# Performance work log

Hardware: AMD Instinct MI355X
Metric: run time of the kernel (lower is better)

Reference implementation:

```python
import jax, jax.numpy as jnp
import numpy as np

B, S, F = 4, 2048, 256
H, D = 8, 32            # n_heads, width_embedding; H*D == F
LN_EPS = 1e-3           # tf.keras LayerNormalization default epsilon


def setup_inputs() -> dict:
    key = jax.random.key(0)
    ks = jax.random.split(key, 6)
    s = 1.0 / np.sqrt(F)
    return {
        "x": jax.random.normal(ks[0], (B, S, F), dtype=jnp.float32),
        "Wq": jax.random.normal(ks[1], (F, H * D), dtype=jnp.float32) * s,
        "Wk": jax.random.normal(ks[2], (F, H * D), dtype=jnp.float32) * s,
        "Wv": jax.random.normal(ks[3], (F, H * D), dtype=jnp.float32) * s,
        "Wf": jax.random.normal(ks[4], (H * D, F), dtype=jnp.float32) * s,
        "bf": jnp.zeros((F,), dtype=jnp.float32),
    }


def reference(x, Wq, Wk, Wv, Wf, bf):
    # QKV projections (no bias), split heads: [B,S,H*D] -> [B,H,S,D]
    def split(t):
        return t.reshape(B, S, H, D).transpose(0, 2, 1, 3)

    q = split(x @ Wq) / jnp.sqrt(jnp.asarray(H, x.dtype))  # NOTE: module scales by sqrt(n_heads)
    k = split(x @ Wk)
    v = split(x @ Wv)

    scores = jnp.einsum("bhsd,bhtd->bhst", q, k)          # [B,H,S,S]
    attn = jax.nn.softmax(scores, axis=-1)
    ctx = jnp.einsum("bhst,bhtd->bhsd", attn, v)           # [B,H,S,D]

    y = ctx.transpose(0, 2, 1, 3).reshape(B, S, H * D)     # merge heads
    y = jax.nn.relu(y @ Wf + bf)                            # final dense with relu

    # residual + LayerNorm(center=False, scale=False)
    z = x + y
    mean = jnp.mean(z, axis=-1, keepdims=True)
    var = jnp.var(z, axis=-1, keepdims=True)
    return (z - mean) * jax.lax.rsqrt(var + LN_EPS)
```

## Files before the change

kernel.cpp:

```cpp
#include <hip/hip_runtime.h>
#include <math.h>

#define NB 4
#define NS 2048
#define NF 256
#define NH 8
#define ND 32

constexpr float LN_EPS = 1e-3f;
constexpr float QSCALE = 0.35355339059327373f;
constexpr float LOG2E  = 1.4426950408889634f;

typedef __bf16 bf16x8 __attribute__((ext_vector_type(8)));
typedef float f32x4 __attribute__((ext_vector_type(4)));

__global__ __launch_bounds__(256)
void prep_w(const float* __restrict__ Wq, const float* __restrict__ Wk,
            const float* __restrict__ Wv, const float* __restrict__ Wf,
            unsigned short* __restrict__ wt)
{
    __shared__ float tile[64][65];
    const int wid = blockIdx.x;
    const int t = threadIdx.x;
    const int z = wid >> 4;
    const int tl = wid & 15;
    const float* W = (z == 0) ? Wq : (z == 1) ? Wk : (z == 2) ? Wv : Wf;
    const float scale = (z == 0) ? QSCALE * LOG2E : 1.0f;
    const int r0 = (tl >> 2) * 64, c0 = (tl & 3) * 64;
    const int tr = t >> 4, tc4 = (t & 15) * 4;

    #pragma unroll
    for (int p = 0; p < 4; ++p) {
        float4 v = *(const float4*)(W + (size_t)(r0 + tr + p * 16) * NF + c0 + tc4);
        tile[tr + p * 16][tc4 + 0] = v.x;
        tile[tr + p * 16][tc4 + 1] = v.y;
        tile[tr + p * 16][tc4 + 2] = v.z;
        tile[tr + p * 16][tc4 + 3] = v.w;
    }
    __syncthreads();
    #pragma unroll
    for (int p = 0; p < 4; ++p) {
        union { ushort4 u; __bf16 h[4]; } o;
        #pragma unroll
        for (int j = 0; j < 4; ++j)
            o.h[j] = (__bf16)(tile[tc4 + j][tr + p * 16] * scale);
        *(ushort4*)(wt + (size_t)z * 65536 + (size_t)(c0 + tr + p * 16) * NF + r0 + tc4) = o.u;
    }
}

__global__ __launch_bounds__(256)
void qkv_mfma(const float* __restrict__ x, const unsigned short* __restrict__ wt,
              unsigned short* __restrict__ qo, unsigned short* __restrict__ ko,
              unsigned short* __restrict__ vo)
{
    const int z = blockIdx.y;
    unsigned short* out = (z == 0) ? qo : (z == 1) ? ko : vo;
    const unsigned short* W = wt + (size_t)z * 65536;

    const int r0 = blockIdx.x * 32;
    const int t = threadIdx.x;
    const int w = t >> 6, lane = t & 63;
    const int l15 = lane & 15, lhi = lane >> 4;
    const int wr = w >> 1, wc = w & 1;

    f32x4 acc[8] = {};

    #pragma unroll 2
    for (int kt = 0; kt < NF; kt += 32) {
        const float* xr = x + (size_t)(r0 + wr * 16 + l15) * NF + kt + lhi * 8;
        float4 f0 = *(const float4*)xr;
        float4 f1 = *(const float4*)(xr + 4);
        bf16x8 a;
        a[0] = (__bf16)f0.x; a[1] = (__bf16)f0.y; a[2] = (__bf16)f0.z; a[3] = (__bf16)f0.w;
        a[4] = (__bf16)f1.x; a[5] = (__bf16)f1.y; a[6] = (__bf16)f1.z; a[7] = (__bf16)f1.w;
        #pragma unroll
        for (int c = 0; c < 8; ++c) {
            bf16x8 b = *(const bf16x8*)(W + (size_t)(wc * 128 + c * 16 + l15) * NF + kt + lhi * 8);
            acc[c] = __builtin_amdgcn_mfma_f32_16x16x32_bf16(a, b, acc[c], 0, 0, 0);
        }
    }

    #pragma unroll
    for (int c = 0; c < 8; ++c) {
        const int col = wc * 128 + c * 16 + l15;
        const int h = col >> 5, d = col & 31;
        #pragma unroll
        for (int r = 0; r < 4; ++r) {
            const int row = r0 + wr * 16 + lhi * 4 + r;
            const int b = row >> 11, s = row & 2047;
            __bf16 o = (__bf16)acc[c][r];
            out[((size_t)(b * NH + h) * NS + s) * ND + d] = *(unsigned short*)&o;
        }
    }
}

__global__ __launch_bounds__(256)
void attn_mfma(const unsigned short* __restrict__ q, const unsigned short* __restrict__ k,
               const unsigned short* __restrict__ v, unsigned short* __restrict__ ctxb)
{
    const int bh = blockIdx.x;
    const int s0 = blockIdx.y * 128;
    const int t = threadIdx.x;
    const int w = t >> 6;
    const int lane = t & 63;
    const int l15 = lane & 15;
    const int lhi = lane >> 4;
    const int sx  = l15 & 8;
    const int wsx = (w & 1) * 8;

    __shared__ unsigned short ps[4][32][72];
    __shared__ unsigned short vt[2][32][72];

    const unsigned short* qb = q + (size_t)bh * NS * ND;
    const unsigned short* kb = k + (size_t)bh * NS * ND;
    const unsigned short* vb = v + (size_t)bh * NS * ND;

    bf16x8 qf0 = *(const bf16x8*)(qb + (size_t)(s0 + w * 32 + l15) * ND + lhi * 8);
    bf16x8 qf1 = *(const bf16x8*)(qb + (size_t)(s0 + w * 32 + 16 + l15) * ND + lhi * 8);

    float lp0 = 0.f, lp1 = 0.f;
    f32x4 acc00 = {0.f,0.f,0.f,0.f}, acc01 = {0.f,0.f,0.f,0.f};
    f32x4 acc10 = {0.f,0.f,0.f,0.f}, acc11 = {0.f,0.f,0.f,0.f};

    bf16x8 kf[4];
    #pragma unroll
    for (int f = 0; f < 4; ++f)
        kf[f] = *(const bf16x8*)(kb + (size_t)(f * 16 + l15) * ND + lhi * 8);
    {
        bf16x8 vv = *(const bf16x8*)(vb + (size_t)lane * ND + w * 8);
        union { bf16x8 v8; unsigned short s[8]; } u; u.v8 = vv;
        #pragma unroll
        for (int i = 0; i < 8; ++i) vt[0][w * 8 + i][lane ^ wsx] = u.s[i];
    }
    __syncthreads();

    int cur = 0;
    #pragma unroll 2
    for (int tI = 0; tI < 32; ++tI) {
        const int ktn = ((tI + 1) & 31) * 64;
        bf16x8 vv = *(const bf16x8*)(vb + (size_t)(ktn + lane) * ND + w * 8);
        bf16x8 kn[4];
        #pragma unroll
        for (int f = 0; f < 4; ++f)
            kn[f] = *(const bf16x8*)(kb + (size_t)(ktn + f * 16 + l15) * ND + lhi * 8);

        const f32x4 zero = {0.f, 0.f, 0.f, 0.f};
        f32x4 sc0[4], sc1[4];
        __builtin_amdgcn_s_setprio(1);
        #pragma unroll
        for (int f = 0; f < 4; ++f) {
            sc0[f] = __builtin_amdgcn_mfma_f32_16x16x32_bf16(kf[f], qf0, zero, 0, 0, 0);
            sc1[f] = __builtin_amdgcn_mfma_f32_16x16x32_bf16(kf[f], qf1, zero, 0, 0, 0);
        }
        __builtin_amdgcn_s_setprio(0);

        float a0 = 0.f, a1 = 0.f;
        #pragma unroll
        for (int f = 0; f < 4; ++f) {
            float p0 = __builtin_amdgcn_exp2f(sc0[f][0]);
            float p1 = __builtin_amdgcn_exp2f(sc0[f][1]);
            float p2 = __builtin_amdgcn_exp2f(sc0[f][2]);
            float p3 = __builtin_amdgcn_exp2f(sc0[f][3]);
            union { ushort4 u; __bf16 h[4]; } pk;
            pk.h[0] = (__bf16)p0; pk.h[1] = (__bf16)p1;
            pk.h[2] = (__bf16)p2; pk.h[3] = (__bf16)p3;
            *(ushort4*)&ps[w][l15][(f * 16 + lhi * 4) ^ sx] = pk.u;
            a0 += (p0 + p1) + (p2 + p3);
        }
        #pragma unroll
        for (int f = 0; f < 4; ++f) {
            float p0 = __builtin_amdgcn_exp2f(sc1[f][0]);
            float p1 = __builtin_amdgcn_exp2f(sc1[f][1]);
            float p2 = __builtin_amdgcn_exp2f(sc1[f][2]);
            float p3 = __builtin_amdgcn_exp2f(sc1[f][3]);
            union { ushort4 u; __bf16 h[4]; } pk;
            pk.h[0] = (__bf16)p0; pk.h[1] = (__bf16)p1;
            pk.h[2] = (__bf16)p2; pk.h[3] = (__bf16)p3;
            *(ushort4*)&ps[w][16 + l15][(f * 16 + lhi * 4) ^ sx] = pk.u;
            a1 += (p0 + p1) + (p2 + p3);
        }
        lp0 += a0; lp1 += a1;

        __builtin_amdgcn_s_setprio(1);
        #pragma unroll
        for (int c = 0; c < 2; ++c) {
            const int co = (c * 32 + lhi * 8) ^ sx;
            bf16x8 pa0 = *(const bf16x8*)&ps[w][l15][co];
            bf16x8 pa1 = *(const bf16x8*)&ps[w][16 + l15][co];
            bf16x8 vf0 = *(const bf16x8*)&vt[cur][l15][co];
            bf16x8 vf1 = *(const bf16x8*)&vt[cur][16 + l15][co];
            acc00 = __builtin_amdgcn_mfma_f32_16x16x32_bf16(pa0, vf0, acc00, 0, 0, 0);
            acc01 = __builtin_amdgcn_mfma_f32_16x16x32_bf16(pa0, vf1, acc01, 0, 0, 0);
            acc10 = __builtin_amdgcn_mfma_f32_16x16x32_bf16(pa1, vf0, acc10, 0, 0, 0);
            acc11 = __builtin_amdgcn_mfma_f32_16x16x32_bf16(pa1, vf1, acc11, 0, 0, 0);
        }
        __builtin_amdgcn_s_setprio(0);

        {
            union { bf16x8 v8; unsigned short s[8]; } u; u.v8 = vv;
            #pragma unroll
            for (int i = 0; i < 8; ++i) vt[cur ^ 1][w * 8 + i][lane ^ wsx] = u.s[i];
        }
        #pragma unroll
        for (int f = 0; f < 4; ++f) kf[f] = kn[f];
        __syncthreads();
        cur ^= 1;
    }

    lp0 += __shfl_xor(lp0, 16);
    lp0 += __shfl_xor(lp0, 32);
    lp1 += __shfl_xor(lp1, 16);
    lp1 += __shfl_xor(lp1, 32);

    const int b = bh >> 3, h = bh & 7;
    #pragma unroll
    for (int r = 0; r < 4; ++r) {
        float li0 = __shfl(lp0, lhi * 4 + r);
        float li1 = __shfl(lp1, lhi * 4 + r);
        float inv0 = 1.0f / li0;
        float inv1 = 1.0f / li1;
        int row0 = s0 + w * 32 + lhi * 4 + r;
        int row1 = row0 + 16;
        unsigned short* op0 = ctxb + ((size_t)b * NS + row0) * NF + h * ND;
        unsigned short* op1 = ctxb + ((size_t)b * NS + row1) * NF + h * ND;
        __bf16 o00 = (__bf16)(acc00[r] * inv0);
        __bf16 o01 = (__bf16)(acc01[r] * inv0);
        __bf16 o10 = (__bf16)(acc10[r] * inv1);
        __bf16 o11 = (__bf16)(acc11[r] * inv1);
        op0[l15]      = *(unsigned short*)&o00;
        op0[16 + l15] = *(unsigned short*)&o01;
        op1[l15]      = *(unsigned short*)&o10;
        op1[16 + l15] = *(unsigned short*)&o11;
    }
}

__global__ __launch_bounds__(256)
void dense_ln(const unsigned short* __restrict__ ctxb, const unsigned short* __restrict__ wft,
              const float* __restrict__ bfp, const float* __restrict__ x,
              float* __restrict__ out)
{
    const int r0 = blockIdx.x * 32;
    const int t = threadIdx.x;
    const int w = t >> 6;
    const int lane = t & 63;
    const int l15 = lane & 15;
    const int lhi = lane >> 4;

    __shared__ float zs[32][258];

    f32x4 acc[2][4] = {};

    #pragma unroll 2
    for (int kt = 0; kt < NF; kt += 32) {
        bf16x8 a0 = *(const bf16x8*)(ctxb + (size_t)(r0 + l15) * NF + kt + lhi * 8);
        bf16x8 a1 = *(const bf16x8*)(ctxb + (size_t)(r0 + 16 + l15) * NF + kt + lhi * 8);
        #pragma unroll
        for (int c = 0; c < 4; ++c) {
            bf16x8 b = *(const bf16x8*)(wft + (size_t)(w * 64 + c * 16 + l15) * NF + kt + lhi * 8);
            acc[0][c] = __builtin_amdgcn_mfma_f32_16x16x32_bf16(a0, b, acc[0][c], 0, 0, 0);
            acc[1][c] = __builtin_amdgcn_mfma_f32_16x16x32_bf16(a1, b, acc[1][c], 0, 0, 0);
        }
    }

    #pragma unroll
    for (int i = 0; i < 2; ++i) {
        #pragma unroll
        for (int c = 0; c < 4; ++c) {
            const int col = w * 64 + c * 16 + l15;
            const float bb = bfp[col];
            #pragma unroll
            for (int r = 0; r < 4; ++r) {
                const int row = i * 16 + lhi * 4 + r;
                zs[row][col] = fmaxf(acc[i][c][r] + bb, 0.0f);
            }
        }
    }
    __syncthreads();

    #pragma unroll
    for (int i = 0; i < 8; ++i) {
        const int row = w * 8 + i;
        float4 yv = *(const float4*)&zs[row][lane * 4];
        float4 xv = *(const float4*)(x + (size_t)(r0 + row) * NF + lane * 4);
        float z0 = xv.x + yv.x, z1 = xv.y + yv.y;
        float z2 = xv.z + yv.z, z3 = xv.w + yv.w;
        float sum = z0 + z1 + z2 + z3;
        float sq  = z0*z0 + z1*z1 + z2*z2 + z3*z3;
        #pragma unroll
        for (int o = 1; o < 64; o <<= 1) {
            sum += __shfl_xor(sum, o);
            sq  += __shfl_xor(sq, o);
        }
        float mean = sum * (1.0f / NF);
        float var  = sq * (1.0f / NF) - mean * mean;
        float rstd = rsqrtf(var + LN_EPS);
        float4 o4;
        o4.x = (z0 - mean) * rstd;
        o4.y = (z1 - mean) * rstd;
        o4.z = (z2 - mean) * rstd;
        o4.w = (z3 - mean) * rstd;
        *(float4*)(out + (size_t)(r0 + row) * NF + lane * 4) = o4;
    }
}

extern "C" void kernel_launch(void* const* d_in, const int* in_sizes, int n_in,
                              void* d_out, int out_size, void* d_ws, size_t ws_size,
                              hipStream_t stream)
{
    const float* x  = (const float*)d_in[0];
    const float* Wq = (const float*)d_in[1];
    const float* Wk = (const float*)d_in[2];
    const float* Wv = (const float*)d_in[3];
    const float* Wf = (const float*)d_in[4];
    const float* bf = (const float*)d_in[5];
    float* out = (float*)d_out;

    const size_t per = (size_t)NB * NH * NS * ND;
    unsigned short* q    = (unsigned short*)d_ws;
    unsigned short* kk   = q + per;
    unsigned short* vv   = kk + per;
    unsigned short* wt   = vv + per;
    unsigned short* ctxb = wt + 4 * 65536;

    prep_w<<<dim3(64), 256, 0, stream>>>(Wq, Wk, Wv, Wf, wt);
    qkv_mfma<<<dim3(256, 3), 256, 0, stream>>>(x, wt, q, kk, vv);
    attn_mfma<<<dim3(NB * NH, NS / 128), 256, 0, stream>>>(q, kk, vv, ctxb);
    dense_ln<<<dim3((NB * NS) / 32), 256, 0, stream>>>(ctxb, wt + 3 * 65536, bf, x, out);
}
```

Measured before the change: 87.14 us.

## Split attention over key range and combine partials; enlarge QKV row tile

Splits the attention key range in two across a third grid dimension so twice as many blocks run. Each block writes unnormalized fp32 partial outputs and row sums, and a new combine kernel merges them and writes the bf16 context. Because the softmax uses no running max (exp2 on scaled scores), the partials can simply be added. The QKV projection also now computes 64 rows per block instead of 32, which halves that grid and reuses each weight fragment across two MFMAs. The cost is an extra kernel launch plus fp32 partial-output traffic to and from memory.

```diff
diff --git a/kernel.cpp b/kernel.cpp
--- a/kernel.cpp
+++ b/kernel.cpp
@@ -10,6 +10,9 @@
 constexpr float LN_EPS = 1e-3f;
 constexpr float QSCALE = 0.35355339059327373f;
 constexpr float LOG2E  = 1.4426950408889634f;
+constexpr int   NSPLIT = 2;
+constexpr int   KRANGE = NS / NSPLIT;
+constexpr size_t PO_PER = (size_t)NB * NH * NS * ND;
 
 typedef __bf16 bf16x8 __attribute__((ext_vector_type(8)));
 typedef float f32x4 __attribute__((ext_vector_type(4)));
@@ -57,49 +60,61 @@
     unsigned short* out = (z == 0) ? qo : (z == 1) ? ko : vo;
     const unsigned short* W = wt + (size_t)z * 65536;
 
-    const int r0 = blockIdx.x * 32;
+    const int r0 = blockIdx.x * 64;
     const int t = threadIdx.x;
     const int w = t >> 6, lane = t & 63;
     const int l15 = lane & 15, lhi = lane >> 4;
     const int wr = w >> 1, wc = w & 1;
 
-    f32x4 acc[8] = {};
+    f32x4 acc[2][8] = {};
 
     #pragma unroll 2
     for (int kt = 0; kt < NF; kt += 32) {
-        const float* xr = x + (size_t)(r0 + wr * 16 + l15) * NF + kt + lhi * 8;
-        float4 f0 = *(const float4*)xr;
-        float4 f1 = *(const float4*)(xr + 4);
-        bf16x8 a;
-        a[0] = (__bf16)f0.x; a[1] = (__bf16)f0.y; a[2] = (__bf16)f0.z; a[3] = (__bf16)f0.w;
-        a[4] = (__bf16)f1.x; a[5] = (__bf16)f1.y; a[6] = (__bf16)f1.z; a[7] = (__bf16)f1.w;
+        const float* xr0 = x + (size_t)(r0 + wr * 32 + l15) * NF + kt + lhi * 8;
+        const float* xr1 = x + (size_t)(r0 + wr * 32 + 16 + l15) * NF + kt + lhi * 8;
+        float4 f00 = *(const float4*)xr0;
+        float4 f01 = *(const float4*)(xr0 + 4);
+        float4 f10 = *(const float4*)xr1;
+        float4 f11 = *(const float4*)(xr1 + 4);
+        bf16x8 a0, a1;
+        a0[0] = (__bf16)f00.x; a0[1] = (__bf16)f00.y; a0[2] = (__bf16)f00.z; a0[3] = (__bf16)f00.w;
+        a0[4] = (__bf16)f01.x; a0[5] = (__bf16)f01.y; a0[6] = (__bf16)f01.z; a0[7] = (__bf16)f01.w;
+        a1[0] = (__bf16)f10.x; a1[1] = (__bf16)f10.y; a1[2] = (__bf16)f10.z; a1[3] = (__bf16)f10.w;
+        a1[4] = (__bf16)f11.x; a1[5] = (__bf16)f11.y; a1[6] = (__bf16)f11.z; a1[7] = (__bf16)f11.w;
         #pragma unroll
         for (int c = 0; c < 8; ++c) {
             bf16x8 b = *(const bf16x8*)(W + (size_t)(wc * 128 + c * 16 + l15) * NF + kt + lhi * 8);
-            acc[c] = __builtin_amdgcn_mfma_f32_16x16x32_bf16(a, b, acc[c], 0, 0, 0);
-        }
-    }
-
-    #pragma unroll
-    for (int c = 0; c < 8; ++c) {
-        const int col = wc * 128 + c * 16 + l15;
-        const int h = col >> 5, d = col & 31;
-        #pragma unroll
-        for (int r = 0; r < 4; ++r) {
-            const int row = r0 + wr * 16 + lhi * 4 + r;
-            const int b = row >> 11, s = row & 2047;
-            __bf16 o = (__bf16)acc[c][r];
-            out[((size_t)(b * NH + h) * NS + s) * ND + d] = *(unsigned short*)&o;
+            acc[0][c] = __builtin_amdgcn_mfma_f32_16x16x32_bf16(a0, b, acc[0][c], 0, 0, 0);
+            acc[1][c] = __builtin_amdgcn_mfma_f32_16x16x32_bf16(a1, b, acc[1][c], 0, 0, 0);
+        }
+    }
+
+    #pragma unroll
+    for (int i = 0; i < 2; ++i) {
+        #pragma unroll
+        for (int c = 0; c < 8; ++c) {
+            const int col = wc * 128 + c * 16 + l15;
+            const int h = col >> 5, d = col & 31;
+            #pragma unroll
+            for (int r = 0; r < 4; ++r) {
+                const int row = r0 + wr * 32 + i * 16 + lhi * 4 + r;
+                const int b = row >> 11, s = row & 2047;
+                __bf16 o = (__bf16)acc[i][c][r];
+                out[((size_t)(b * NH + h) * NS + s) * ND + d] = *(unsigned short*)&o;
+            }
         }
     }
 }
 
 __global__ __launch_bounds__(256)
 void attn_mfma(const unsigned short* __restrict__ q, const unsigned short* __restrict__ k,
-               const unsigned short* __restrict__ v, unsigned short* __restrict__ ctxb)
+               const unsigned short* __restrict__ v, float* __restrict__ po,
+               float* __restrict__ pl)
 {
     const int bh = blockIdx.x;
     const int s0 = blockIdx.y * 128;
+    const int sp = blockIdx.z;
+    const int kbase = sp * KRANGE;
     const int t = threadIdx.x;
     const int w = t >> 6;
     const int lane = t & 63;
@@ -125,9 +140,9 @@
     bf16x8 kf[4];
     #pragma unroll
     for (int f = 0; f < 4; ++f)
-        kf[f] = *(const bf16x8*)(kb + (size_t)(f * 16 + l15) * ND + lhi * 8);
+        kf[f] = *(const bf16x8*)(kb + (size_t)(kbase + f * 16 + l15) * ND + lhi * 8);
     {
-        bf16x8 vv = *(const bf16x8*)(vb + (size_t)lane * ND + w * 8);
+        bf16x8 vv = *(const bf16x8*)(vb + (size_t)(kbase + lane) * ND + w * 8);
         union { bf16x8 v8; unsigned short s[8]; } u; u.v8 = vv;
         #pragma unroll
         for (int i = 0; i < 8; ++i) vt[0][w * 8 + i][lane ^ wsx] = u.s[i];
@@ -136,8 +151,8 @@
 
     int cur = 0;
     #pragma unroll 2
-    for (int tI = 0; tI < 32; ++tI) {
-        const int ktn = ((tI + 1) & 31) * 64;
+    for (int tI = 0; tI < 16; ++tI) {
+        const int ktn = kbase + ((tI + 1) & 15) * 64;
         bf16x8 vv = *(const bf16x8*)(vb + (size_t)(ktn + lane) * ND + w * 8);
         bf16x8 kn[4];
         #pragma unroll
@@ -212,26 +227,55 @@
     lp1 += __shfl_xor(lp1, 16);
     lp1 += __shfl_xor(lp1, 32);
 
-    const int b = bh >> 3, h = bh & 7;
+    float* pob = po + (size_t)sp * PO_PER;
+    float* plb = pl + (size_t)sp * (NB * NH * NS);
     #pragma unroll
     for (int r = 0; r < 4; ++r) {
         float li0 = __shfl(lp0, lhi * 4 + r);
         float li1 = __shfl(lp1, lhi * 4 + r);
-        float inv0 = 1.0f / li0;
-        float inv1 = 1.0f / li1;
         int row0 = s0 + w * 32 + lhi * 4 + r;
         int row1 = row0 + 16;
-        unsigned short* op0 = ctxb + ((size_t)b * NS + row0) * NF + h * ND;
-        unsigned short* op1 = ctxb + ((size_t)b * NS + row1) * NF + h * ND;
-        __bf16 o00 = (__bf16)(acc00[r] * inv0);
-        __bf16 o01 = (__bf16)(acc01[r] * inv0);
-        __bf16 o10 = (__bf16)(acc10[r] * inv1);
-        __bf16 o11 = (__bf16)(acc11[r] * inv1);
-        op0[l15]      = *(unsigned short*)&o00;
-        op0[16 + l15] = *(unsigned short*)&o01;
-        op1[l15]      = *(unsigned short*)&o10;
-        op1[16 + l15] = *(unsigned short*)&o11;
-    }
+        float* op0 = pob + ((size_t)bh * NS + row0) * ND;
+        float* op1 = pob + ((size_t)bh * NS + row1) * ND;
+        op0[l15]      = acc00[r];
+        op0[16 + l15] = acc01[r];
+        op1[l15]      = acc10[r];
+        op1[16 + l15] = acc11[r];
+        if (l15 == 0) {
+            plb[bh * NS + row0] = li0;
+            plb[bh * NS + row1] = li1;
+        }
+    }
+}
+
+__global__ __launch_bounds__(256)
+void combine(const float* __restrict__ po, const float* __restrict__ pl,
+             unsigned short* __restrict__ ctxb)
+{
+    const int idx = blockIdx.x * 256 + threadIdx.x;
+    const int row = idx >> 2;
+    const int dd = (idx & 3) * 8;
+    const float* p0 = po + (size_t)row * ND + dd;
+    const float* p1 = p0 + PO_PER;
+    float inv = 1.0f / (pl[row] + pl[row + NB * NH * NS]);
+    float4 a0 = *(const float4*)p0;
+    float4 a1 = *(const float4*)(p0 + 4);
+    float4 b0 = *(const float4*)p1;
+    float4 b1 = *(const float4*)(p1 + 4);
+    union { ushort4 u[2]; __bf16 h[8]; } o;
+    o.h[0] = (__bf16)((a0.x + b0.x) * inv);
+    o.h[1] = (__bf16)((a0.y + b0.y) * inv);
+    o.h[2] = (__bf16)((a0.z + b0.z) * inv);
+    o.h[3] = (__bf16)((a0.w + b0.w) * inv);
+    o.h[4] = (__bf16)((a1.x + b1.x) * inv);
+    o.h[5] = (__bf16)((a1.y + b1.y) * inv);
+    o.h[6] = (__bf16)((a1.z + b1.z) * inv);
+    o.h[7] = (__bf16)((a1.w + b1.w) * inv);
+    const int bh = row >> 11, s = row & 2047;
+    const int b = bh >> 3, h = bh & 7;
+    unsigned short* op = ctxb + ((size_t)b * NS + s) * NF + h * ND + dd;
+    *(ushort4*)op = o.u[0];
+    *(ushort4*)(op + 4) = o.u[1];
 }
 
 __global__ __launch_bounds__(256)
@@ -321,9 +365,12 @@
     unsigned short* vv   = kk + per;
     unsigned short* wt   = vv + per;
     unsigned short* ctxb = wt + 4 * 65536;
+    float* po = (float*)(ctxb + per);
+    float* pl = po + (size_t)NSPLIT * PO_PER;
 
     prep_w<<<dim3(64), 256, 0, stream>>>(Wq, Wk, Wv, Wf, wt);
-    qkv_mfma<<<dim3(256, 3), 256, 0, stream>>>(x, wt, q, kk, vv);
-    attn_mfma<<<dim3(NB * NH, NS / 128), 256, 0, stream>>>(q, kk, vv, ctxb);
+    qkv_mfma<<<dim3(128, 3), 256, 0, stream>>>(x, wt, q, kk, vv);
+    attn_mfma<<<dim3(NB * NH, NS / 128, NSPLIT), 256, 0, stream>>>(q, kk, vv, po, pl);
+    combine<<<dim3((NB * NS * NF / 8) / 256), 256, 0, stream>>>(po, pl, ctxb);
     dense_ln<<<dim3((NB * NS) / 32), 256, 0, stream>>>(ctxb, wt + 3 * 65536, bf, x, out);
 }
```

Result: faster. 85.20 us (-2.2%).
